# Kernel optimization log

Hardware: AMD Instinct MI355X
Metric: run time of the kernel (lower is better)

Reference implementation:

```python
import jax, jax.numpy as jnp
import numpy as np

D_MODEL = 512
N_HEADS = 8
D_K = 64
D_V = 64
SCALE = 1.0 / np.sqrt(D_K).astype(np.float32)
LN_EPS = 1e-5


def setup_inputs() -> dict:
    key = jax.random.key(0)
    ks = jax.random.split(key, 8)
    B, S = 4, 2048
    xavier = np.sqrt(6.0 / (D_MODEL + D_MODEL)).astype(np.float32)
    return {
        "input_Q": jax.random.normal(ks[0], (B, S, D_MODEL), jnp.float32),
        "input_K": jax.random.normal(ks[1], (B, S, D_MODEL), jnp.float32),
        "input_V": jax.random.normal(ks[2], (B, S, D_MODEL), jnp.float32),
        "attn_mask": jax.random.randint(ks[3], (B, S, S), 0, 2).astype(bool),
        "W_Q": jax.random.uniform(ks[4], (D_MODEL, D_MODEL), jnp.float32, -xavier, xavier),
        "W_K": jax.random.uniform(ks[5], (D_MODEL, D_MODEL), jnp.float32, -xavier, xavier),
        "W_V": jax.random.uniform(ks[6], (D_MODEL, D_MODEL), jnp.float32, -xavier, xavier),
        "W_fc": jax.random.uniform(ks[7], (D_MODEL, D_MODEL), jnp.float32, -xavier, xavier),
        "ln_gamma": jnp.ones((D_MODEL,), jnp.float32),
        "ln_beta": jnp.zeros((D_MODEL,), jnp.float32),
    }


def _layernorm(x, gamma, beta):
    mu = jnp.mean(x, axis=-1, keepdims=True)
    var = jnp.mean(jnp.square(x - mu), axis=-1, keepdims=True)
    return (x - mu) * jax.lax.rsqrt(var + LN_EPS) * gamma + beta


def reference(input_Q, input_K, input_V, attn_mask, W_Q, W_K, W_V, W_fc, ln_gamma, ln_beta):
    B = input_Q.shape[0]
    # torch Linear: x @ W.T ; W is (out, in)
    def proj(x, W):
        y = jnp.einsum('bsd,ed->bse', x, W)  # (B,S,n_heads*d_k)
        return y.reshape(B, -1, N_HEADS, D_K).transpose(0, 2, 1, 3)  # (B,H,S,dk)

    Q = proj(input_Q, W_Q)
    K = proj(input_K, W_K)
    V = proj(input_V, W_V)

    scores = jnp.einsum('bhqd,bhkd->bhqk', Q, K) * SCALE
    scores = jnp.clip(scores, -1e9, 1e10)
    mask = attn_mask[:, None, :, :]  # broadcast over heads
    scores = jnp.where(mask, jnp.float32(-1e9), scores)
    attn = jax.nn.softmax(scores, axis=-1)
    attn = jnp.clip(attn, 1e-8, 1.0)
    result = jnp.einsum('bhqk,bhkd->bhqd', attn, V)
    result = result.transpose(0, 2, 1, 3).reshape(B, -1, N_HEADS * D_V)
    output = jnp.einsum('bsd,ed->bse', result, W_fc)
    out = _layernorm(output + input_Q, ln_gamma, ln_beta)
    return (out, attn)
```

## Files before the change

### kernel.cpp

```cpp
#include <hip/hip_runtime.h>

typedef float  f32x4  __attribute__((ext_vector_type(4)));
typedef __bf16 bf16x8 __attribute__((ext_vector_type(8)));

#define MFMA_BF16(a, b, c) __builtin_amdgcn_mfma_f32_16x16x32_bf16((a), (b), (c), 0, 0, 0)

#define BDIM   4
#define SEQ    2048
#define DM     512
#define NH     8
#define DK     64
#define ATT_SCALE 0.125f
#define NEG_CAP  (-80.0f)
#define KT     64
#define NT     (SEQ / KT)
#define QB     128
#define PS     72
#define KTDK   (KT * DK)

static __device__ __forceinline__ unsigned short f2bf(float f) {
  unsigned int u = __builtin_bit_cast(unsigned int, f);
  u += 0x7fffu + ((u >> 16) & 1u);
  return (unsigned short)(u >> 16);
}
static __device__ __forceinline__ float bf2f(unsigned short u) {
  return __builtin_bit_cast(float, (unsigned)u << 16);
}
static __device__ __forceinline__ void gload16(const void* g, unsigned short* l) {
  __builtin_amdgcn_global_load_lds((const __attribute__((address_space(1))) void*)g,
                                   (__attribute__((address_space(3))) void*)l, 16, 0, 0);
}
static __device__ __forceinline__ bf16x8 lds128(const unsigned short* base, int row, int m) {
  return *(const bf16x8*)((const char*)base + row * 128 + (((m) ^ (row & 7)) << 4));
}

__global__ __launch_bounds__(256) void cvt7_kernel(
    const float* __restrict__ x0, const float* __restrict__ x1, const float* __restrict__ x2,
    const float* __restrict__ w0, const float* __restrict__ w1, const float* __restrict__ w2,
    const float* __restrict__ w3,
    unsigned short* __restrict__ dx0, unsigned short* __restrict__ dx1,
    unsigned short* __restrict__ dx2, unsigned short* __restrict__ dw0,
    unsigned short* __restrict__ dw1, unsigned short* __restrict__ dw2,
    unsigned short* __restrict__ dw3, int nx4, int nw4) {
  const int z = blockIdx.y;
  const float* src;
  unsigned short* dst;
  int n4;
  switch (z) {
    case 0: src = x0; dst = dx0; n4 = nx4; break;
    case 1: src = x1; dst = dx1; n4 = nx4; break;
    case 2: src = x2; dst = dx2; n4 = nx4; break;
    case 3: src = w0; dst = dw0; n4 = nw4; break;
    case 4: src = w1; dst = dw1; n4 = nw4; break;
    case 5: src = w2; dst = dw2; n4 = nw4; break;
    default: src = w3; dst = dw3; n4 = nw4; break;
  }
  int i = blockIdx.x * 256 + threadIdx.x;
  if (i >= n4) return;
  float4 v = reinterpret_cast<const float4*>(src)[i];
  ushort4 o;
  o.x = f2bf(v.x); o.y = f2bf(v.y); o.z = f2bf(v.z); o.w = f2bf(v.w);
  reinterpret_cast<ushort4*>(dst)[i] = o;
}

__global__ void detect_mask_kernel(const unsigned int* __restrict__ m, int* __restrict__ flag) {
  __shared__ int s;
  if (threadIdx.x == 0) s = 0;
  __syncthreads();
  int any = 0;
  for (int i = threadIdx.x; i < 4096; i += 256) any |= (m[i] > 1u) ? 1 : 0;
  if (any) atomicOr(&s, 1);
  __syncthreads();
  if (threadIdx.x == 0) *flag = s;
}

__global__ __launch_bounds__(256) void mask_pack_kernel(const unsigned char* __restrict__ m8,
                                                        const int* __restrict__ m32,
                                                        const int* __restrict__ flag,
                                                        unsigned long long* __restrict__ bits) {
  const int wid = blockIdx.x * 256 + threadIdx.x;
  const int use8 = *flag;
  unsigned long long v = 0;
  if (use8) {
    const uchar4* p = (const uchar4*)(m8 + (size_t)wid * 64);
#pragma unroll
    for (int c = 0; c < 16; ++c) {
      uchar4 q = p[c];
      v |= ((unsigned long long)(q.x != 0)) << (c * 4 + 0);
      v |= ((unsigned long long)(q.y != 0)) << (c * 4 + 1);
      v |= ((unsigned long long)(q.z != 0)) << (c * 4 + 2);
      v |= ((unsigned long long)(q.w != 0)) << (c * 4 + 3);
    }
  } else {
    const int4* p = (const int4*)(m32 + (size_t)wid * 64);
#pragma unroll
    for (int c = 0; c < 16; ++c) {
      int4 q = p[c];
      v |= ((unsigned long long)(q.x != 0)) << (c * 4 + 0);
      v |= ((unsigned long long)(q.y != 0)) << (c * 4 + 1);
      v |= ((unsigned long long)(q.z != 0)) << (c * 4 + 2);
      v |= ((unsigned long long)(q.w != 0)) << (c * 4 + 3);
    }
  }
  bits[wid] = v;
}

__device__ __forceinline__ void gemm128_main(const unsigned short* __restrict__ A,
                                             const unsigned short* __restrict__ B,
                                             int K, int row0, int col0,
                                             unsigned short* lds, f32x4 acc[4][4]) {
  const int tid  = threadIdx.x;
  const int w    = tid >> 6;
  const int lane = tid & 63;
  const int lr   = lane & 15;
  const int lk   = (lane >> 4) << 3;
  const int wm   = (w >> 1) << 6;
  const int wn   = (w & 1) << 6;
  const int sr   = tid >> 2;
  const int sc   = (tid & 3) << 3;
  unsigned short* As = lds;
  unsigned short* Bs = lds + 128 * 40;
  for (int k0 = 0; k0 < K; k0 += 32) {
    __syncthreads();
    *(int4*)&As[(size_t)sr * 40 + sc]        = *(const int4*)&A[(size_t)(row0 + sr) * K + k0 + sc];
    *(int4*)&As[(size_t)(sr + 64) * 40 + sc] = *(const int4*)&A[(size_t)(row0 + sr + 64) * K + k0 + sc];
    *(int4*)&Bs[(size_t)sr * 40 + sc]        = *(const int4*)&B[(size_t)(col0 + sr) * K + k0 + sc];
    *(int4*)&Bs[(size_t)(sr + 64) * 40 + sc] = *(const int4*)&B[(size_t)(col0 + sr + 64) * K + k0 + sc];
    __syncthreads();
    bf16x8 af[4], bfr[4];
#pragma unroll
    for (int mi = 0; mi < 4; ++mi) af[mi]  = *(const bf16x8*)&As[(size_t)(wm + mi * 16 + lr) * 40 + lk];
#pragma unroll
    for (int ni = 0; ni < 4; ++ni) bfr[ni] = *(const bf16x8*)&Bs[(size_t)(wn + ni * 16 + lr) * 40 + lk];
#pragma unroll
    for (int mi = 0; mi < 4; ++mi)
#pragma unroll
      for (int ni = 0; ni < 4; ++ni)
        acc[mi][ni] = MFMA_BF16(af[mi], bfr[ni], acc[mi][ni]);
  }
}

__global__ __launch_bounds__(256) void proj_kernel(
    const unsigned short* __restrict__ Xq, const unsigned short* __restrict__ Xk,
    const unsigned short* __restrict__ Xv,
    const unsigned short* __restrict__ Wq, const unsigned short* __restrict__ Wk,
    const unsigned short* __restrict__ Wv,
    unsigned short* __restrict__ Qh, unsigned short* __restrict__ Kh,
    unsigned short* __restrict__ VT) {
  __shared__ __align__(16) unsigned short lds[2 * 128 * 40];
  const int z = blockIdx.z;
  const unsigned short* A = (z == 0) ? Xq : ((z == 1) ? Xk : Xv);
  const unsigned short* B = (z == 0) ? Wq : ((z == 1) ? Wk : Wv);
  unsigned short* O       = (z == 0) ? Qh : ((z == 1) ? Kh : VT);
  const int row0 = blockIdx.x * 128, col0 = blockIdx.y * 128;
  f32x4 acc[4][4];
  const f32x4 zero = {0.f, 0.f, 0.f, 0.f};
#pragma unroll
  for (int mi = 0; mi < 4; ++mi)
#pragma unroll
    for (int ni = 0; ni < 4; ++ni) acc[mi][ni] = zero;
  gemm128_main(A, B, DM, row0, col0, lds, acc);
  const int w = threadIdx.x >> 6, lane = threadIdx.x & 63;
  const int lr = lane & 15, lg = lane >> 4;
  const int wm = (w >> 1) << 6, wn = (w & 1) << 6;
#pragma unroll
  for (int mi = 0; mi < 4; ++mi)
#pragma unroll
    for (int ni = 0; ni < 4; ++ni)
#pragma unroll
      for (int j = 0; j < 4; ++j) {
        const int m = row0 + wm + mi * 16 + lg * 4 + j;
        const int n = col0 + wn + ni * 16 + lr;
        const int b = m >> 11, s = m & 2047;
        const int h = n >> 6,  d = n & 63;
        const unsigned short val = f2bf(acc[mi][ni][j]);
        if (z == 2)
          O[(((size_t)(b * NH + h)) * DK + d) * SEQ + s] = val;
        else
          O[(((size_t)(b * NH + h)) * SEQ + s) * DK + d] = val;
      }
}

__global__ __launch_bounds__(256) void fc_kernel(const unsigned short* __restrict__ A,
                                                 const unsigned short* __restrict__ W,
                                                 float* __restrict__ Out) {
  __shared__ __align__(16) unsigned short lds[2 * 128 * 40];
  const int row0 = blockIdx.x * 128, col0 = blockIdx.y * 128;
  f32x4 acc[4][4];
  const f32x4 zero = {0.f, 0.f, 0.f, 0.f};
#pragma unroll
  for (int mi = 0; mi < 4; ++mi)
#pragma unroll
    for (int ni = 0; ni < 4; ++ni) acc[mi][ni] = zero;
  gemm128_main(A, W, DM, row0, col0, lds, acc);
  const int w = threadIdx.x >> 6, lane = threadIdx.x & 63;
  const int lr = lane & 15, lg = lane >> 4;
  const int wm = (w >> 1) << 6, wn = (w & 1) << 6;
#pragma unroll
  for (int mi = 0; mi < 4; ++mi)
#pragma unroll
    for (int ni = 0; ni < 4; ++ni)
#pragma unroll
      for (int j = 0; j < 4; ++j) {
        const int m = row0 + wm + mi * 16 + lg * 4 + j;
        const int n = col0 + wn + ni * 16 + lr;
        Out[(size_t)m * DM + n] = acc[mi][ni][j];
      }
}

__global__ __launch_bounds__(512, 4) void attn_kernel(
    const unsigned short* __restrict__ Qh, const unsigned short* __restrict__ Kh,
    const unsigned short* __restrict__ VT, const unsigned long long* __restrict__ Mb,
    float* __restrict__ attn_out, unsigned short* __restrict__ R16) {
  __shared__ __align__(16) unsigned short Ks[2][KTDK];
  __shared__ __align__(16) unsigned short Vs[2][KTDK];
  __shared__ __align__(16) unsigned short Pl[2][8][16 * PS];
  const int id  = blockIdx.x + 16 * (blockIdx.y + 8 * blockIdx.z);
  const int q8  = id >> 3;
  const int bh  = (id & 7) * 4 + (q8 >> 4);
  const int qt  = q8 & 15;
  const int b   = bh >> 3;
  const int tid = threadIdx.x, w = tid >> 6, lane = tid & 63;
  const int lr = lane & 15, lg = lane >> 4;
  const unsigned short* Qp = Qh + (size_t)bh * SEQ * DK;
  const unsigned short* Kp = Kh + (size_t)bh * SEQ * DK;
  const unsigned short* Vp = VT + (size_t)bh * DK * SEQ;
  float* ap = attn_out + (size_t)bh * SEQ * SEQ;

  const int qb = qt * QB + w * 16;
  const bf16x8 qf0 = *(const bf16x8*)(Qp + (size_t)(qb + lr) * DK + lg * 8);
  const bf16x8 qf1 = *(const bf16x8*)(Qp + (size_t)(qb + lr) * DK + 32 + lg * 8);
  const unsigned long long* mrow = Mb + ((size_t)b * SEQ + qb + lr) * 32;

  const int srow = tid >> 3, schunk = tid & 7;
  const int sg = schunk ^ (srow & 7);
  const unsigned short* kstage = Kp + (size_t)srow * DK + sg * 8;
  const unsigned short* vstage = Vp + (size_t)srow * SEQ + sg * 8;
  unsigned short* kdst0 = &Ks[0][tid * 8];
  unsigned short* kdst1 = &Ks[1][tid * 8];
  unsigned short* vdst0 = &Vs[0][tid * 8];
  unsigned short* vdst1 = &Vs[1][tid * 8];

  float sv[4][4];

  float l = 0.f;
  gload16(kstage, kdst0);
  __syncthreads();
  for (int t = 0; t < NT; ++t) {
    const unsigned short* Kb = Ks[t & 1];
    if (t + 1 < NT) gload16(kstage + (size_t)(t + 1) * KTDK, (t & 1) ? kdst0 : kdst1);
    const unsigned long long mr = mrow[t];
#pragma unroll
    for (int ni = 0; ni < 4; ++ni) {
      const int r = ni * 16 + lr;
      bf16x8 k0 = lds128(Kb, r, lg);
      bf16x8 k1 = lds128(Kb, r, lg + 4);
      f32x4 z = {0.f, 0.f, 0.f, 0.f};
      z = MFMA_BF16(k0, qf0, z);
      z = MFMA_BF16(k1, qf1, z);
#pragma unroll
      for (int j = 0; j < 4; ++j)
        sv[ni][j] = ((mr >> (ni * 16 + lg * 4 + j)) & 1ull) ? NEG_CAP : z[j] * ATT_SCALE;
    }
#pragma unroll
    for (int ni = 0; ni < 4; ++ni)
      l += __expf(sv[ni][0]) + __expf(sv[ni][1]) + __expf(sv[ni][2]) + __expf(sv[ni][3]);
    __syncthreads();
  }
  l += __shfl_xor(l, 16);
  l += __shfl_xor(l, 32);
  const float invl = 1.0f / l;

  f32x4 o[4];
  const f32x4 zero = {0.f, 0.f, 0.f, 0.f};
#pragma unroll
  for (int nd = 0; nd < 4; ++nd) o[nd] = zero;
  unsigned short* Pw0 = &Pl[0][w][0];
  unsigned short* Pw1 = &Pl[1][w][0];

  gload16(kstage, kdst0);
  gload16(vstage, vdst0);
  __syncthreads();
  for (int t = 0; t < NT; ++t) {
    const unsigned short* Kb = Ks[t & 1];
    const unsigned short* Vb = Vs[t & 1];
    unsigned short* PwCur  = (t & 1) ? Pw1 : Pw0;
    unsigned short* PwPrev = (t & 1) ? Pw0 : Pw1;
    if (t + 1 < NT) {
      gload16(kstage + (size_t)(t + 1) * KTDK, (t & 1) ? kdst0 : kdst1);
      gload16(vstage + (size_t)(t + 1) * KT,   (t & 1) ? vdst0 : vdst1);
    }
    const unsigned long long mr = mrow[t];
#pragma unroll
    for (int ni = 0; ni < 4; ++ni) {
      const int r = ni * 16 + lr;
      bf16x8 k0 = lds128(Kb, r, lg);
      bf16x8 k1 = lds128(Kb, r, lg + 4);
      f32x4 z = {0.f, 0.f, 0.f, 0.f};
      z = MFMA_BF16(k0, qf0, z);
      z = MFMA_BF16(k1, qf1, z);
#pragma unroll
      for (int j = 0; j < 4; ++j)
        sv[ni][j] = ((mr >> (ni * 16 + lg * 4 + j)) & 1ull) ? NEG_CAP : z[j] * ATT_SCALE;
    }
    if (t > 0) {
#pragma unroll
      for (int j = 0; j < 4; ++j) {
        const int r = lg * 4 + j;
        ushort4 pk = *(const ushort4*)&PwPrev[r * PS + lr * 4];
        float4 f = {bf2f(pk.x), bf2f(pk.y), bf2f(pk.z), bf2f(pk.w)};
        *(float4*)(ap + (size_t)(qb + r) * SEQ + (t - 1) * KT + lr * 4) = f;
      }
    }
#pragma unroll
    for (int ni = 0; ni < 4; ++ni) {
      float p0 = fminf(fmaxf(__expf(sv[ni][0]) * invl, 1e-8f), 1.0f);
      float p1 = fminf(fmaxf(__expf(sv[ni][1]) * invl, 1e-8f), 1.0f);
      float p2 = fminf(fmaxf(__expf(sv[ni][2]) * invl, 1e-8f), 1.0f);
      float p3 = fminf(fmaxf(__expf(sv[ni][3]) * invl, 1e-8f), 1.0f);
      ushort4 pk = {f2bf(p0), f2bf(p1), f2bf(p2), f2bf(p3)};
      *(ushort4*)&PwCur[lr * PS + ni * 16 + lg * 4] = pk;
    }
    const bf16x8 pf0 = *(const bf16x8*)&PwCur[lr * PS + lg * 8];
    const bf16x8 pf1 = *(const bf16x8*)&PwCur[lr * PS + 32 + lg * 8];
#pragma unroll
    for (int nd = 0; nd < 4; ++nd) {
      const int r = nd * 16 + lr;
      o[nd] = MFMA_BF16(pf0, lds128(Vb, r, lg), o[nd]);
    }
#pragma unroll
    for (int nd = 0; nd < 4; ++nd) {
      const int r = nd * 16 + lr;
      o[nd] = MFMA_BF16(pf1, lds128(Vb, r, lg + 4), o[nd]);
    }
    __syncthreads();
  }
  {
    unsigned short* PwLast = ((NT - 1) & 1) ? Pw1 : Pw0;
#pragma unroll
    for (int j = 0; j < 4; ++j) {
      const int r = lg * 4 + j;
      ushort4 pk = *(const ushort4*)&PwLast[r * PS + lr * 4];
      float4 f = {bf2f(pk.x), bf2f(pk.y), bf2f(pk.z), bf2f(pk.w)};
      *(float4*)(ap + (size_t)(qb + r) * SEQ + (NT - 1) * KT + lr * 4) = f;
    }
  }
#pragma unroll
  for (int nd = 0; nd < 4; ++nd)
#pragma unroll
    for (int j = 0; j < 4; ++j)
      R16[((size_t)(b * SEQ + qb + lg * 4 + j)) * DM + (bh & 7) * DK + nd * 16 + lr] = f2bf(o[nd][j]);
}

__global__ __launch_bounds__(256) void ln_kernel(const float* __restrict__ fc,
                                                 const float* __restrict__ xq,
                                                 const float* __restrict__ gamma,
                                                 const float* __restrict__ beta,
                                                 float* __restrict__ out) {
  const int row = blockIdx.x * 4 + (threadIdx.x >> 6);
  const int lane = threadIdx.x & 63;
  const float* f = fc + (size_t)row * DM;
  const float* x = xq + (size_t)row * DM;
  float v[8];
  float s = 0.f, ss = 0.f;
#pragma unroll
  for (int i = 0; i < 8; ++i) {
    const int c = lane + i * 64;
    const float t = f[c] + x[c];
    v[i] = t; s += t; ss += t * t;
  }
#pragma unroll
  for (int off = 1; off < 64; off <<= 1) {
    s  += __shfl_xor(s, off);
    ss += __shfl_xor(ss, off);
  }
  const float mu  = s * (1.f / 512.f);
  const float var = ss * (1.f / 512.f) - mu * mu;
  const float inv = rsqrtf(var + 1e-5f);
  float* op = out + (size_t)row * DM;
#pragma unroll
  for (int i = 0; i < 8; ++i) {
    const int c = lane + i * 64;
    op[c] = (v[i] - mu) * inv * gamma[c] + beta[c];
  }
}


extern "C" void kernel_launch(void* const* d_in, const int* in_sizes, int n_in,
                              void* d_out, int out_size, void* d_ws, size_t ws_size,
                              hipStream_t stream) {
  const float* xq   = (const float*)d_in[0];
  const float* xk   = (const float*)d_in[1];
  const float* xv   = (const float*)d_in[2];
  const void*  mask = d_in[3];
  const float* wq   = (const float*)d_in[4];
  const float* wk   = (const float*)d_in[5];
  const float* wv   = (const float*)d_in[6];
  const float* wfc  = (const float*)d_in[7];
  const float* gamma = (const float*)d_in[8];
  const float* beta  = (const float*)d_in[9];

  float* out = (float*)d_out;
  float* attn_out = out + (size_t)BDIM * SEQ * DM;

  char* ws = (char*)d_ws;
  unsigned short* XQ16 = (unsigned short*)(ws);
  unsigned short* XK16 = (unsigned short*)(ws + 8388608);
  unsigned short* XV16 = (unsigned short*)(ws + 16777216);
  unsigned short* WQ16 = (unsigned short*)(ws + 25165824);
  unsigned short* WK16 = (unsigned short*)(ws + 25690112);
  unsigned short* WV16 = (unsigned short*)(ws + 26214400);
  unsigned short* WF16 = (unsigned short*)(ws + 26738688);
  unsigned short* Qh   = (unsigned short*)(ws + 27262976);
  unsigned short* Kh   = (unsigned short*)(ws + 35651584);
  unsigned short* VT   = (unsigned short*)(ws + 44040192);
  unsigned long long* Mbits = (unsigned long long*)(ws);
  unsigned short* R16  = (unsigned short*)(ws + 16777216);
  float*          FC32 = (float*)(ws + 27262976);
  int*            FLAG = (int*)(ws + 52428800);

  const int NX4 = BDIM * SEQ * DM / 4;
  const int NW4 = DM * DM / 4;

  detect_mask_kernel<<<1, 256, 0, stream>>>((const unsigned int*)mask, FLAG);
  cvt7_kernel<<<dim3(NX4 / 256, 7), 256, 0, stream>>>(xq, xk, xv, wq, wk, wv, wfc,
                                                      XQ16, XK16, XV16,
                                                      WQ16, WK16, WV16, WF16, NX4, NW4);
  proj_kernel<<<dim3(64, 4, 3), 256, 0, stream>>>(XQ16, XK16, XV16,
                                                  WQ16, WK16, WV16, Qh, Kh, VT);
  mask_pack_kernel<<<1024, 256, 0, stream>>>((const unsigned char*)mask,
                                             (const int*)mask, FLAG, Mbits);
  attn_kernel<<<dim3(16, NH, BDIM), 512, 0, stream>>>(Qh, Kh, VT, Mbits, attn_out, R16);
  fc_kernel<<<dim3(64, 4, 1), 256, 0, stream>>>(R16, WF16, FC32);
  ln_kernel<<<2048, 256, 0, stream>>>(FC32, xq, gamma, beta, out);
}
```

Before: 309.8 us.

## Single-buffer P tile and replace syncthreads with partial vmcnt barrier

Drops the double-buffered per-wave P staging tile and writes the attention probabilities for the current tile right after the PV MFMAs instead of one iteration late. The full __syncthreads at the end of each iteration becomes a raw s_barrier preceded by s_waitcnt vmcnt(4), so the global stores of attn_out no longer have to drain before the next tile starts. This cuts LDS use and barrier stalls. The vmcnt count depends on exactly how many memory ops are outstanding (the K/V prefetch loads versus the attn stores). If that assumption is wrong, the K/V LDS writes may not be visible when the next tile reads them.

Measured after the change: 309.8 us. Within noise of the previous version (-0.0%).

```diff
diff --git a/kernel.cpp b/kernel.cpp
--- a/kernel.cpp
+++ b/kernel.cpp
@@ -214,7 +214,7 @@
     float* __restrict__ attn_out, unsigned short* __restrict__ R16) {
   __shared__ __align__(16) unsigned short Ks[2][KTDK];
   __shared__ __align__(16) unsigned short Vs[2][KTDK];
-  __shared__ __align__(16) unsigned short Pl[2][8][16 * PS];
+  __shared__ __align__(16) unsigned short Pl[8][16 * PS];
   const int id  = blockIdx.x + 16 * (blockIdx.y + 8 * blockIdx.z);
   const int q8  = id >> 3;
   const int bh  = (id & 7) * 4 + (q8 >> 4);
@@ -275,17 +275,15 @@
   const f32x4 zero = {0.f, 0.f, 0.f, 0.f};
 #pragma unroll
   for (int nd = 0; nd < 4; ++nd) o[nd] = zero;
-  unsigned short* Pw0 = &Pl[0][w][0];
-  unsigned short* Pw1 = &Pl[1][w][0];
+  unsigned short* Pw = &Pl[w][0];
 
   gload16(kstage, kdst0);
   gload16(vstage, vdst0);
-  __syncthreads();
+  asm volatile("s_waitcnt vmcnt(0)" ::: "memory");
+  __builtin_amdgcn_s_barrier();
   for (int t = 0; t < NT; ++t) {
     const unsigned short* Kb = Ks[t & 1];
     const unsigned short* Vb = Vs[t & 1];
-    unsigned short* PwCur  = (t & 1) ? Pw1 : Pw0;
-    unsigned short* PwPrev = (t & 1) ? Pw0 : Pw1;
     if (t + 1 < NT) {
       gload16(kstage + (size_t)(t + 1) * KTDK, (t & 1) ? kdst0 : kdst1);
       gload16(vstage + (size_t)(t + 1) * KT,   (t & 1) ? vdst0 : vdst1);
@@ -303,15 +301,6 @@
       for (int j = 0; j < 4; ++j)
         sv[ni][j] = ((mr >> (ni * 16 + lg * 4 + j)) & 1ull) ? NEG_CAP : z[j] * ATT_SCALE;
     }
-    if (t > 0) {
-#pragma unroll
-      for (int j = 0; j < 4; ++j) {
-        const int r = lg * 4 + j;
-        ushort4 pk = *(const ushort4*)&PwPrev[r * PS + lr * 4];
-        float4 f = {bf2f(pk.x), bf2f(pk.y), bf2f(pk.z), bf2f(pk.w)};
-        *(float4*)(ap + (size_t)(qb + r) * SEQ + (t - 1) * KT + lr * 4) = f;
-      }
-    }
 #pragma unroll
     for (int ni = 0; ni < 4; ++ni) {
       float p0 = fminf(fmaxf(__expf(sv[ni][0]) * invl, 1e-8f), 1.0f);
@@ -319,10 +308,10 @@
       float p2 = fminf(fmaxf(__expf(sv[ni][2]) * invl, 1e-8f), 1.0f);
       float p3 = fminf(fmaxf(__expf(sv[ni][3]) * invl, 1e-8f), 1.0f);
       ushort4 pk = {f2bf(p0), f2bf(p1), f2bf(p2), f2bf(p3)};
-      *(ushort4*)&PwCur[lr * PS + ni * 16 + lg * 4] = pk;
-    }
-    const bf16x8 pf0 = *(const bf16x8*)&PwCur[lr * PS + lg * 8];
-    const bf16x8 pf1 = *(const bf16x8*)&PwCur[lr * PS + 32 + lg * 8];
+      *(ushort4*)&Pw[lr * PS + ni * 16 + lg * 4] = pk;
+    }
+    const bf16x8 pf0 = *(const bf16x8*)&Pw[lr * PS + lg * 8];
+    const bf16x8 pf1 = *(const bf16x8*)&Pw[lr * PS + 32 + lg * 8];
 #pragma unroll
     for (int nd = 0; nd < 4; ++nd) {
       const int r = nd * 16 + lr;
@@ -333,16 +322,16 @@
       const int r = nd * 16 + lr;
       o[nd] = MFMA_BF16(pf1, lds128(Vb, r, lg + 4), o[nd]);
     }
-    __syncthreads();
-  }
-  {
-    unsigned short* PwLast = ((NT - 1) & 1) ? Pw1 : Pw0;
 #pragma unroll
     for (int j = 0; j < 4; ++j) {
       const int r = lg * 4 + j;
-      ushort4 pk = *(const ushort4*)&PwLast[r * PS + lr * 4];
+      ushort4 pk = *(const ushort4*)&Pw[r * PS + lr * 4];
       float4 f = {bf2f(pk.x), bf2f(pk.y), bf2f(pk.z), bf2f(pk.w)};
-      *(float4*)(ap + (size_t)(qb + r) * SEQ + (NT - 1) * KT + lr * 4) = f;
+      *(float4*)(ap + (size_t)(qb + r) * SEQ + t * KT + lr * 4) = f;
+    }
+    if (t + 1 < NT) {
+      asm volatile("s_waitcnt vmcnt(4)" ::: "memory");
+      __builtin_amdgcn_s_barrier();
     }
   }
 #pragma unroll
```
